# Kernel optimization log

Measured on AMD Instinct MI355X. Metric: run time of the kernel, lower is better.

## Reference

```python
import jax, jax.numpy as jnp
import numpy as np

NUM_HEADS = 16


def setup_inputs() -> dict:
    key = jax.random.key(0)
    ks = jax.random.split(key, 8)
    B, N, C = 2, 1024, 1024
    H, D = NUM_HEADS, C // NUM_HEADS
    Npast = 8192
    s = 0.02
    return {
        "x": jax.random.normal(ks[0], (B, N, C), jnp.float32),
        "past_k": jax.random.normal(ks[1], (B, H, Npast, D), jnp.float32),
        "past_v": jax.random.normal(ks[2], (B, H, Npast, D), jnp.float32),
        "qkv_w": jax.random.normal(ks[3], (3 * C, C), jnp.float32) * s,
        "qkv_b": jax.random.normal(ks[4], (3 * C,), jnp.float32) * s,
        "proj_w": jax.random.normal(ks[5], (C, C), jnp.float32) * s,
        "proj_b": jax.random.normal(ks[6], (C,), jnp.float32) * s,
        "cache_budget": 4096,
    }


def reference(x, past_k, past_v, qkv_w, qkv_b, proj_w, proj_b, cache_budget):
    B, N, C = x.shape
    H = NUM_HEADS
    D = C // H
    scale = D ** -0.5

    # fused QKV projection -> [3, B, H, N, D]
    qkv = (x @ qkv_w.T + qkv_b).reshape(B, N, 3, H, D).transpose(2, 0, 3, 1, 4)
    q, k, v = qkv[0], qkv[1], qkv[2]

    # use_cache path: anchor tokens = current-frame token count on first call
    num_anchor = N
    k = jnp.concatenate([past_k, k], axis=2)  # [B,H,Ntot,D]
    v = jnp.concatenate([past_v, v], axis=2)
    Ntot = k.shape[2]

    # eviction: mean cosine-similarity scoring over candidate (non-anchor) keys.
    # mean_j cos(k_i, k_j) == khat_i . mean_j(khat_j) -- O(N*D), no NxN matrix.
    num_keep = cache_budget - num_anchor
    cand_k = k[:, :, num_anchor:, :]  # [B,H,Ncand,D]
    khat = cand_k / (jnp.linalg.norm(cand_k, axis=-1, keepdims=True) + 1e-6)
    mean_dir = khat.mean(axis=2, keepdims=True)
    mean_scores = (khat * mean_dir).sum(-1)  # [B,H,Ncand]
    # keep the least-redundant tokens (lowest mean similarity)
    _, top_idx = jax.lax.top_k(-mean_scores, num_keep)  # [B,H,num_keep]
    top_idx = jnp.sort(top_idx, axis=-1)
    avg_scores = mean_scores.mean()

    anchor_idx = jnp.broadcast_to(jnp.arange(num_anchor)[None, None, :], (B, H, num_anchor))
    keep_idx = jnp.concatenate([anchor_idx, top_idx + num_anchor], axis=2)  # [B,H,budget]
    gidx = keep_idx[..., None]
    k_new = jnp.take_along_axis(k, jnp.broadcast_to(gidx, (B, H, cache_budget, D)), axis=2)
    v_new = jnp.take_along_axis(v, jnp.broadcast_to(gidx, (B, H, cache_budget, D)), axis=2)

    # SDPA
    logits = jnp.einsum("bhqd,bhkd->bhqk", q, k_new) * scale
    attn = jax.nn.softmax(logits, axis=-1)
    o = jnp.einsum("bhqk,bhkd->bhqd", attn, v_new)
    o = o.transpose(0, 2, 1, 3).reshape(B, N, C)
    out = o @ proj_w.T + proj_b
    return out, k_new, v_new, avg_scores
```

## Files before the change

### kernel.cpp

```cpp
#include <hip/hip_runtime.h>
#include <hip/hip_bf16.h>
#include <math.h>

#define BB 2
#define HH 16
#define NN 1024
#define CC 1024
#define DD 64
#define NPAST 8192
#define NANCH 1024
#define CBUD 4096
#define NKEEP 3072
#define NCAND 8192
#define BH 32

#define TILEB 16384

#define OUT_SZ   (BB*NN*CC)
#define KNEW_OFF ((size_t)OUT_SZ)
#define KNEW_SZ  ((size_t)BH*CBUD*DD)
#define VNEW_OFF (KNEW_OFF + KNEW_SZ)
#define AVG_OFF  (VNEW_OFF + KNEW_SZ)

#define WS_KF   ((size_t)0)
#define WS_VF   ((size_t)2097152)
#define WS_VTS  ((size_t)0)
#define WS_XT   ((size_t)4194304)
#define WS_OT   ((size_t)4194304)
#define WS_WQVT ((size_t)5242880)
#define WS_WPT  ((size_t)5242880)
#define WS_QB   ((size_t)6291456)
#define WS_MD   ((size_t)7340032)
#define WS_SC   ((size_t)7342080)
#define WS_BS   ((size_t)7604224)
#define WS_SEL  ((size_t)7604288)
#define WS_MDP  ((size_t)7702592)
#define WS_BSP  ((size_t)7718976)
#define WS_KTS  ((size_t)7719232)

typedef __attribute__((ext_vector_type(8))) short short8;
typedef __attribute__((ext_vector_type(4))) float f32x4;

typedef unsigned int __attribute__((address_space(3))) lds_uint;
typedef unsigned int __attribute__((address_space(1))) glb_uint;

__device__ __forceinline__ void gload16(const void* g, void* l) {
    __builtin_amdgcn_global_load_lds((const glb_uint*)g, (lds_uint*)l, 16, 0, 0);
}

__device__ inline unsigned short f2bf(float f) {
    unsigned u = __float_as_uint(f);
    unsigned r = (u + 0x7FFFu + ((u >> 16) & 1u)) >> 16;
    return (unsigned short)r;
}
__device__ inline unsigned cvtpk(float a, float b) {
    __hip_bfloat162 h = __float22bfloat162_rn(make_float2(a, b));
    return *reinterpret_cast<unsigned*>(&h);
}
__device__ __forceinline__ float fexp2(float x) {
#if __has_builtin(__builtin_amdgcn_exp2f)
    return __builtin_amdgcn_exp2f(x);
#else
    return exp2f(x);
#endif
}

__global__ __launch_bounds__(256) void kf_conv(const float* __restrict__ x,
                                               const float* __restrict__ qw,
                                               const float* __restrict__ bias,
                                               float* __restrict__ ws,
                                               unsigned short* __restrict__ xt,
                                               unsigned short* __restrict__ wqvt)
{
    __shared__ float As[2][16][68];
    __shared__ float Bs[2][16][68];
    int bid = blockIdx.x;
    int tid = threadIdx.x;

    if (bid >= 512) {
        int cb = bid - 512;
        int gid = (cb & 1023) * 256 + tid;
        int r = gid >> 7, k0 = (gid & 127) * 8;
        const float* src;
        unsigned short* dst;
        int srow;
        if (cb < 1024) { src = x;  dst = xt;   srow = r; }
        else           { src = qw; dst = wqvt; srow = (r < 1024) ? r : r + 1024; }
        float4 a = *(const float4*)&src[(size_t)srow * 1024 + k0];
        float4 b = *(const float4*)&src[(size_t)srow * 1024 + k0 + 4];
        uint4 u;
        u.x = cvtpk(a.x, a.y); u.y = cvtpk(a.z, a.w);
        u.z = cvtpk(b.x, b.y); u.w = cvtpk(b.z, b.w);
        size_t tile = (size_t)(r >> 7) * 16 + (k0 >> 6);
        int inner = (((r & 127) * 128 + (k0 & 63) * 2)) ^ ((r & 7) << 4);
        *(uint4*)((char*)dst + tile * TILEB + inner) = u;
        return;
    }

    int m0 = (bid >> 4) * 64;
    int n0 = (bid & 15) * 64;
    int tx = tid & 15, ty = tid >> 4;
    int lr = tid >> 2;
    int lk = (tid & 3) * 4;
    float acc[4][4] = {{0.f}};

    {
        float4 a = *(const float4*)&x[(size_t)(m0 + lr) * CC + lk];
        float4 b = *(const float4*)&qw[(size_t)(1024 + n0 + lr) * CC + lk];
        As[0][lk+0][lr] = a.x; As[0][lk+1][lr] = a.y; As[0][lk+2][lr] = a.z; As[0][lk+3][lr] = a.w;
        Bs[0][lk+0][lr] = b.x; Bs[0][lk+1][lr] = b.y; Bs[0][lk+2][lr] = b.z; Bs[0][lk+3][lr] = b.w;
    }
    __syncthreads();

    int cur = 0;
    for (int k0 = 0; k0 < CC; k0 += 16) {
        float4 a, b;
        bool more = (k0 + 16 < CC);
        if (more) {
            a = *(const float4*)&x[(size_t)(m0 + lr) * CC + k0 + 16 + lk];
            b = *(const float4*)&qw[(size_t)(1024 + n0 + lr) * CC + k0 + 16 + lk];
        }
        float tacc[4][4] = {{0.f}};
        #pragma unroll
        for (int kk = 0; kk < 16; ++kk) {
            float4 a4 = *(const float4*)&As[cur][kk][ty*4];
            float4 b4 = *(const float4*)&Bs[cur][kk][tx*4];
            float av[4] = {a4.x, a4.y, a4.z, a4.w};
            float bv[4] = {b4.x, b4.y, b4.z, b4.w};
            #pragma unroll
            for (int i = 0; i < 4; ++i)
                #pragma unroll
                for (int j = 0; j < 4; ++j)
                    tacc[i][j] += av[i] * bv[j];
        }
        #pragma unroll
        for (int i = 0; i < 4; ++i)
            #pragma unroll
            for (int j = 0; j < 4; ++j)
                acc[i][j] += tacc[i][j];
        if (more) {
            As[cur^1][lk+0][lr] = a.x; As[cur^1][lk+1][lr] = a.y;
            As[cur^1][lk+2][lr] = a.z; As[cur^1][lk+3][lr] = a.w;
            Bs[cur^1][lk+0][lr] = b.x; Bs[cur^1][lk+1][lr] = b.y;
            Bs[cur^1][lk+2][lr] = b.z; Bs[cur^1][lk+3][lr] = b.w;
        }
        __syncthreads();
        cur ^= 1;
    }

    int cn0 = n0 + tx * 4;
    int h = cn0 >> 6, dd0 = cn0 & 63;
    float4 b4 = *(const float4*)&bias[1024 + cn0];
    float* kf = ws + WS_KF;
    #pragma unroll
    for (int i = 0; i < 4; ++i) {
        int m = m0 + ty * 4 + i;
        int b2 = m >> 10, n = m & 1023;
        float4 t;
        t.x = acc[i][0] + b4.x; t.y = acc[i][1] + b4.y;
        t.z = acc[i][2] + b4.z; t.w = acc[i][3] + b4.w;
        *(float4*)&kf[(((size_t)b2*HH + h)*NN + n)*DD + dd0] = t;
    }
}

template<int MODE>
__global__ __launch_bounds__(256) void mfma_gemm(const unsigned short* __restrict__ At,
                                                 const unsigned short* __restrict__ Bt,
                                                 const float* __restrict__ bias,
                                                 float* __restrict__ outp)
{
    __shared__ char lds[131072];
    int tid = threadIdx.x;
    int w = tid >> 6, lane = tid & 63;
    int g = lane >> 4, r16 = lane & 15;
    int wr = w >> 1, wc = w & 1;
    int bm = blockIdx.y, bn = blockIdx.x;
    const int KB = 16;
    const float QSCL = 0.125f * 1.44269504089f;

    f32x4 acc[4][4];
    #pragma unroll
    for (int i = 0; i < 4; ++i)
        #pragma unroll
        for (int j = 0; j < 4; ++j) acc[i][j] = 0.f;

    const char* Abase = (const char*)At + (size_t)bm * KB * TILEB;
    const char* Bbase = (const char*)Bt + (size_t)bn * KB * TILEB;

    #pragma unroll
    for (int i = 0; i < 4; ++i) {
        gload16(Abase + (size_t)w*4096 + i*1024 + lane*16, lds + w*4096 + i*1024);
        gload16(Bbase + (size_t)w*4096 + i*1024 + lane*16, lds + TILEB + w*4096 + i*1024);
    }
    asm volatile("s_waitcnt vmcnt(0)" ::: "memory");
    __syncthreads();

    int cur = 0;
    for (int kb = 0; kb < KB; ++kb) {
        char* Acur = lds + cur * (2*TILEB);
        char* Bcur = Acur + TILEB;
        if (kb + 1 < KB) {
            char* Anxt = lds + (cur ^ 1) * (2*TILEB);
            char* Bnxt = Anxt + TILEB;
            const char* an = Abase + (size_t)(kb+1)*TILEB + w*4096;
            const char* bsrc = Bbase + (size_t)(kb+1)*TILEB + w*4096;
            #pragma unroll
            for (int i = 0; i < 4; ++i) {
                gload16(an + i*1024 + lane*16, Anxt + w*4096 + i*1024);
                gload16(bsrc + i*1024 + lane*16, Bnxt + w*4096 + i*1024);
            }
        }
        short8 a0[4], a1[4], b0[4], b1[4];
        #pragma unroll
        for (int mi = 0; mi < 4; ++mi) {
            int row = wr*64 + mi*16 + r16;
            int sw = (row & 7) << 4;
            a0[mi] = *(const short8*)(Acur + ((row*128 + g*16) ^ sw));
            a1[mi] = *(const short8*)(Acur + ((row*128 + 64 + g*16) ^ sw));
        }
        #pragma unroll
        for (int ni = 0; ni < 4; ++ni) {
            int row = wc*64 + ni*16 + r16;
            int sw = (row & 7) << 4;
            b0[ni] = *(const short8*)(Bcur + ((row*128 + g*16) ^ sw));
            b1[ni] = *(const short8*)(Bcur + ((row*128 + 64 + g*16) ^ sw));
        }
        __builtin_amdgcn_s_setprio(1);
        #pragma unroll
        for (int mi = 0; mi < 4; ++mi)
            #pragma unroll
            for (int ni = 0; ni < 4; ++ni) {
                acc[mi][ni] = __builtin_amdgcn_mfma_f32_16x16x32_bf16(a0[mi], b0[ni], acc[mi][ni], 0, 0, 0);
                acc[mi][ni] = __builtin_amdgcn_mfma_f32_16x16x32_bf16(a1[mi], b1[ni], acc[mi][ni], 0, 0, 0);
            }
        __builtin_amdgcn_s_setprio(0);
        asm volatile("s_waitcnt vmcnt(0)" ::: "memory");
        __syncthreads();
        cur ^= 1;
    }

    int nq = bn*128 + wc*64;
    float bv[4];
    #pragma unroll
    for (int ni = 0; ni < 4; ++ni) {
        int n = nq + ni*16 + r16;
        bv[ni] = (MODE == 0) ? bias[(n < 1024) ? n : (n + 1024)] : bias[n];
    }
    #pragma unroll
    for (int mi = 0; mi < 4; ++mi) {
        #pragma unroll
        for (int rr = 0; rr < 4; ++rr) {
            int ml = wr*64 + mi*16 + 4*g + rr;
            int mg = bm*128 + ml;
            int bb = mg >> 10, tok = mg & 1023;
            #pragma unroll
            for (int ni = 0; ni < 4; ++ni) {
                int n = nq + ni*16 + r16;
                float v = acc[mi][ni][rr] + bv[ni];
                if (MODE == 0) {
                    if (n < 1024) {
                        unsigned short* qb = (unsigned short*)(outp + WS_QB);
                        int hh = n >> 6, d = n & 63;
                        qb[(((size_t)bb*16 + hh)*1024 + tok)*64 + d] = f2bf(v * QSCL);
                    } else {
                        float* vf = outp + WS_VF;
                        int hh = (n - 1024) >> 6, d = n & 63;
                        vf[(((size_t)bb*16 + hh)*1024 + tok)*64 + d] = v;
                    }
                } else {
                    outp[(size_t)mg*1024 + n] = v;
                }
            }
        }
    }
}

__global__ __launch_bounds__(256) void meandir_part(const float* __restrict__ past_k,
                                                    float* __restrict__ ws)
{
    int bh = blockIdx.x, seg = blockIdx.y, tid = threadIdx.x;
    const float* kpast = past_k + (size_t)bh * NPAST * DD;
    const float* knew  = ws + WS_KF + (size_t)bh * NN * DD;
    float dir[64];
    #pragma unroll
    for (int i = 0; i < 64; ++i) dir[i] = 0.f;

    int j0 = seg * 1024;
    for (int jj = tid; jj < 1024; jj += 256) {
        int pos = NANCH + j0 + jj;
        const float* row = (pos < NPAST) ? (kpast + (size_t)pos * DD)
                                         : (knew + (size_t)(pos - NPAST) * DD);
        float v[64]; float ss = 0.f;
        #pragma unroll
        for (int g = 0; g < 16; ++g) {
            float4 t = *(const float4*)&row[g*4];
            v[4*g]=t.x; v[4*g+1]=t.y; v[4*g+2]=t.z; v[4*g+3]=t.w;
            ss += t.x*t.x + t.y*t.y + t.z*t.z + t.w*t.w;
        }
        float inv = 1.0f / (sqrtf(ss) + 1e-6f);
        #pragma unroll
        for (int i = 0; i < 64; ++i) dir[i] += v[i] * inv;
    }
    #pragma unroll
    for (int i = 0; i < 64; ++i)
        for (int off = 32; off; off >>= 1) dir[i] += __shfl_xor(dir[i], off);

    __shared__ float sdir[4][64];
    int lane = tid & 63, wid = tid >> 6;
    if (lane == 0) {
        #pragma unroll
        for (int i = 0; i < 64; ++i) sdir[wid][i] = dir[i];
    }
    __syncthreads();
    if (tid < 64) {
        float s = sdir[0][tid] + sdir[1][tid] + sdir[2][tid] + sdir[3][tid];
        ws[WS_MDP + ((size_t)bh*8 + seg)*DD + tid] = s;
    }
}

__global__ __launch_bounds__(256) void scores_part(const float* __restrict__ past_k,
                                                   float* __restrict__ ws)
{
    __shared__ float md[64];
    __shared__ float sred[4];
    int bh = blockIdx.x, seg = blockIdx.y, tid = threadIdx.x;
    if (tid < 64) {
        float s = 0.f;
        #pragma unroll
        for (int sg = 0; sg < 8; ++sg)
            s += ws[WS_MDP + ((size_t)bh*8 + sg)*DD + tid];
        md[tid] = s * (1.0f / (float)NCAND);
    }
    __syncthreads();
    const float* kpast = past_k + (size_t)bh * NPAST * DD;
    const float* knew  = ws + WS_KF + (size_t)bh * NN * DD;
    float ssum = 0.f;
    int j0 = seg * 1024;
    for (int jj = tid; jj < 1024; jj += 256) {
        int j = j0 + jj;
        int pos = NANCH + j;
        const float* row = (pos < NPAST) ? (kpast + (size_t)pos * DD)
                                         : (knew + (size_t)(pos - NPAST) * DD);
        float ss = 0.f, dp = 0.f;
        #pragma unroll
        for (int g = 0; g < 16; ++g) {
            float4 t = *(const float4*)&row[g*4];
            ss += t.x*t.x + t.y*t.y + t.z*t.z + t.w*t.w;
            dp += t.x*md[4*g] + t.y*md[4*g+1] + t.z*md[4*g+2] + t.w*md[4*g+3];
        }
        float sc = dp / (sqrtf(ss) + 1e-6f);
        ws[WS_SC + (size_t)bh*NCAND + j] = sc;
        ssum += sc;
    }
    for (int off = 32; off; off >>= 1) ssum += __shfl_xor(ssum, off);
    int lane = tid & 63, wid = tid >> 6;
    if (lane == 0) sred[wid] = ssum;
    __syncthreads();
    if (tid == 0)
        ws[WS_BSP + (size_t)bh*8 + seg] = sred[0] + sred[1] + sred[2] + sred[3];
}

__global__ __launch_bounds__(1024) void topk_k(float* __restrict__ ws, int* __restrict__ sel,
                                               float* __restrict__ dout)
{
    __shared__ unsigned keys[NCAND];
    __shared__ int hist[256];
    __shared__ int red[16];
    __shared__ int red2[16];
    __shared__ float fred[16];
    __shared__ int bcast;
    __shared__ unsigned bbyte;
    int bh = blockIdx.x, tid = threadIdx.x;
    int lane = tid & 63, wid = tid >> 6;

    if (bh == 0) {
        float v = (tid < 256) ? ws[WS_BSP + tid] : 0.f;
        for (int off = 32; off; off >>= 1) v += __shfl_xor(v, off);
        if (lane == 0) fred[wid] = v;
        __syncthreads();
        if (tid == 0) {
            float s = 0.f;
            for (int i = 0; i < 16; ++i) s += fred[i];
            dout[AVG_OFF] = s * (1.0f / ((float)BH * (float)NCAND));
        }
        __syncthreads();
    }

    for (int j = tid; j < NCAND; j += 1024) {
        unsigned u = __float_as_uint(ws[WS_SC + (size_t)bh*NCAND + j]);
        u ^= (u & 0x80000000u) ? 0xFFFFFFFFu : 0x80000000u;
        keys[j] = u;
    }
    __syncthreads();

    int rem = NKEEP;
    unsigned prefix = 0;
    #pragma unroll
    for (int pass = 0; pass < 4; ++pass) {
        int shift = 24 - 8*pass;
        if (tid < 256) hist[tid] = 0;
        __syncthreads();
        unsigned himask = (pass == 0) ? 0u : (0xFFFFFFFFu << (shift + 8));
        for (int j = tid; j < NCAND; j += 1024) {
            unsigned k = keys[j];
            if ((k & himask) == prefix)
                atomicAdd(&hist[(k >> shift) & 255], 1);
        }
        __syncthreads();
        if (tid == 0) {
            int cum = 0, b = 0;
            for (; b < 255; ++b) {
                if (rem <= cum + hist[b]) break;
                cum += hist[b];
            }
            bcast = cum;
            bbyte = (unsigned)b;
        }
        __syncthreads();
        rem -= bcast;
        prefix |= (bbyte << shift);
        __syncthreads();
    }
    unsigned T = prefix;

    {
        int cnt = 0;
        for (int j = tid; j < NCAND; j += 1024) cnt += (int)(keys[j] < T);
        for (int off = 32; off; off >>= 1) cnt += __shfl_xor(cnt, off);
        if (lane == 0) red[wid] = cnt;
        __syncthreads();
        if (tid == 0) { int c = 0; for (int i = 0; i < 16; ++i) c += red[i]; bcast = c; }
        __syncthreads();
    }
    int c_less = bcast;
    int ttie = NKEEP - c_less;

    int base = tid * 8;
    unsigned kv[8]; int lcnt = 0, ecnt = 0;
    #pragma unroll
    for (int i = 0; i < 8; ++i) {
        kv[i] = keys[base + i];
        lcnt += (int)(kv[i] < T);
        ecnt += (int)(kv[i] == T);
    }
    int li = lcnt, ei = ecnt;
    for (int off = 1; off < 64; off <<= 1) {
        int tl = __shfl_up(li, off);
        int te = __shfl_up(ei, off);
        if (lane >= off) { li += tl; ei += te; }
    }
    __syncthreads();
    if (lane == 63) { red[wid] = li; red2[wid] = ei; }
    __syncthreads();
    int lb = 0, eb = 0;
    for (int w = 0; w < wid; ++w) { lb += red[w]; eb += red2[w]; }
    lb += li - lcnt; eb += ei - ecnt;
    #pragma unroll
    for (int i = 0; i < 8; ++i) {
        bool less = kv[i] < T, eq = kv[i] == T;
        if (less || (eq && eb < ttie)) {
            int pos = lb + (eb < ttie ? eb : ttie);
            sel[(size_t)bh*NKEEP + pos] = base + i;
        }
        lb += (int)less; eb += (int)eq;
    }
}

__global__ __launch_bounds__(256) void gather_k(const float* __restrict__ past_k,
                                                const float* __restrict__ past_v,
                                                const float* __restrict__ ws,
                                                const int* __restrict__ sel,
                                                float* __restrict__ dout)
{
    int gid = blockIdx.x * 256 + threadIdx.x;
    int row = gid >> 4, lane = gid & 15;
    int bh = row >> 12, r = row & 4095;
    int pos = (r < NANCH) ? r : (NANCH + sel[(size_t)bh*NKEEP + (r - NANCH)]);
    const float *kr, *vr;
    if (pos < NPAST) {
        kr = past_k + ((size_t)bh*NPAST + pos) * DD;
        vr = past_v + ((size_t)bh*NPAST + pos) * DD;
    } else {
        kr = ws + WS_KF + ((size_t)bh*NN + (pos - NPAST)) * DD;
        vr = ws + WS_VF + ((size_t)bh*NN + (pos - NPAST)) * DD;
    }
    float4 kq = *(const float4*)&kr[lane*4];
    float4 vq = *(const float4*)&vr[lane*4];
    *(float4*)&dout[KNEW_OFF + ((size_t)bh*CBUD + r)*DD + lane*4] = kq;
    *(float4*)&dout[VNEW_OFF + ((size_t)bh*CBUD + r)*DD + lane*4] = vq;
}

__global__ __launch_bounds__(256) void vtrans_conv(const float* __restrict__ dout,
                                                   unsigned short* __restrict__ vt,
                                                   const float* __restrict__ pw,
                                                   unsigned short* __restrict__ wpt,
                                                   unsigned short* __restrict__ ktp,
                                                   int nkblk)
{
    int bid = blockIdx.x;
    if (bid >= 2048 && bid < 2048 + nkblk) {
        int bid2 = bid - 2048;
        int bh = bid2 >> 6, kt = bid2 & 63;
        int tid = threadIdx.x;
        int r = tid >> 2, c4 = (tid & 3) * 16;
        const float* kn = dout + KNEW_OFF + ((size_t)bh*CBUD + kt*64 + r)*DD + c4;
        float4 f0 = *(const float4*)&kn[0];
        float4 f1 = *(const float4*)&kn[4];
        float4 f2 = *(const float4*)&kn[8];
        float4 f3 = *(const float4*)&kn[12];
        uint4 u0, u1;
        u0.x = cvtpk(f0.x,f0.y); u0.y = cvtpk(f0.z,f0.w);
        u0.z = cvtpk(f1.x,f1.y); u0.w = cvtpk(f1.z,f1.w);
        u1.x = cvtpk(f2.x,f2.y); u1.y = cvtpk(f2.z,f2.w);
        u1.z = cvtpk(f3.x,f3.y); u1.w = cvtpk(f3.z,f3.w);
        size_t tbase = ((size_t)bh*64 + kt) * 8192;
        int sw = (r & 7) << 4;
        *(uint4*)((char*)ktp + tbase + ((r*128 + c4*2)      ^ sw)) = u0;
        *(uint4*)((char*)ktp + tbase + ((r*128 + c4*2 + 16) ^ sw)) = u1;
        return;
    }
    if (bid >= 2048 + nkblk) {
        int gid = (bid - 2048 - nkblk) * 256 + threadIdx.x;
        int r = gid >> 7, k0 = (gid & 127) * 8;
        float4 a = *(const float4*)&pw[(size_t)r * 1024 + k0];
        float4 b = *(const float4*)&pw[(size_t)r * 1024 + k0 + 4];
        uint4 u;
        u.x = cvtpk(a.x, a.y); u.y = cvtpk(a.z, a.w);
        u.z = cvtpk(b.x, b.y); u.w = cvtpk(b.z, b.w);
        size_t tile = (size_t)(r >> 7) * 16 + (k0 >> 6);
        int inner = (((r & 127) * 128 + (k0 & 63) * 2)) ^ ((r & 7) << 4);
        *(uint4*)((char*)wpt + tile * TILEB + inner) = u;
        return;
    }
    __shared__ unsigned short S[64][65];
    int bh = bid >> 6, kt = bid & 63;
    int c0 = kt * 64;
    int tid = threadIdx.x;
    int r = tid >> 2, c4 = (tid & 3) * 16;
    const float* src = dout + VNEW_OFF + ((size_t)bh*CBUD + c0 + r)*DD + c4;
    #pragma unroll
    for (int i = 0; i < 4; ++i) {
        float4 f = *(const float4*)&src[i*4];
        S[r][c4 + i*4 + 0] = f2bf(f.x);
        S[r][c4 + i*4 + 1] = f2bf(f.y);
        S[r][c4 + i*4 + 2] = f2bf(f.z);
        S[r][c4 + i*4 + 3] = f2bf(f.w);
    }
    __syncthreads();
    int d = r, k4 = c4;
    uint4 u0, u1;
    u0.x = (unsigned)S[k4+0][d] | ((unsigned)S[k4+1][d] << 16);
    u0.y = (unsigned)S[k4+2][d] | ((unsigned)S[k4+3][d] << 16);
    u0.z = (unsigned)S[k4+4][d] | ((unsigned)S[k4+5][d] << 16);
    u0.w = (unsigned)S[k4+6][d] | ((unsigned)S[k4+7][d] << 16);
    u1.x = (unsigned)S[k4+8][d] | ((unsigned)S[k4+9][d] << 16);
    u1.y = (unsigned)S[k4+10][d] | ((unsigned)S[k4+11][d] << 16);
    u1.z = (unsigned)S[k4+12][d] | ((unsigned)S[k4+13][d] << 16);
    u1.w = (unsigned)S[k4+14][d] | ((unsigned)S[k4+15][d] << 16);
    size_t tbase = ((size_t)bh*64 + kt) * 8192;
    int sw = (d & 7) << 4;
    *(uint4*)((char*)vt + tbase + ((d*128 + k4*2)      ^ sw)) = u0;
    *(uint4*)((char*)vt + tbase + ((d*128 + k4*2 + 16) ^ sw)) = u1;
}

template<int KTS>
__global__ __launch_bounds__(256) void attn_mfma(const unsigned short* __restrict__ qb,
                                                 const float* __restrict__ dout,
                                                 const unsigned short* __restrict__ vt,
                                                 const unsigned short* __restrict__ ktp,
                                                 unsigned short* __restrict__ ot)
{
    __shared__ char kls[2][2][8192];
    __shared__ char vls[2][2][8192];
    __shared__ char pls[4][2048];

    int orig = blockIdx.x;
    int bid = (orig & 7) * 64 + (orig >> 3);
    int bh = bid >> 4, qt = bid & 15;
    int b = bh >> 4, h = bh & 15;
    int tid = threadIdx.x;
    int w = tid >> 6, lane = tid & 63;
    int g = lane >> 4, r16 = lane & 15;
    int q0 = qt * 64 + w * 16;

    const unsigned short* qrow = qb + ((size_t)bh*NN + q0 + r16) * DD;
    short8 qa0 = *(const short8*)&qrow[8*g];
    short8 qa1 = *(const short8*)&qrow[32 + 8*g];

    const float* kf = dout + KNEW_OFF + (size_t)bh * CBUD * DD;
    const char* vtt = (const char*)vt + (size_t)bh * 64 * 8192;
    const char* ktt = (const char*)ktp + (size_t)bh * 64 * 8192;
    char* plw = pls[w];
    int psw = (r16 & 7) << 4;

    int ro[8];
    #pragma unroll
    for (int t4 = 0; t4 < 4; ++t4) {
        int row = 16*t4 + r16;
        ro[2*t4]   = (row*128 + g*16) ^ psw;
        ro[2*t4+1] = (row*128 + 64 + g*16) ^ psw;
    }
    int pwo[4];
    #pragma unroll
    for (int t4 = 0; t4 < 4; ++t4)
        pwo[t4] = (r16*128 + (16*t4 + 4*g)*2) ^ psw;
    int pro0 = (r16*128 + 16*g) ^ psw;
    int pro1 = (r16*128 + 64 + 16*g) ^ psw;

    int srA = tid >> 3, srB = srA + 32;
    int scb = (tid & 7) * 16;
    int d0  = scb >> 1;
    int sdA = (srA*128 + scb) ^ ((srA & 7) << 4);
    int sdB = (srB*128 + scb) ^ ((srB & 7) << 4);

    f32x4 accd[4];
    #pragma unroll
    for (int dt = 0; dt < 4; ++dt) accd[dt] = 0.f;
    float lsum = 0.f;
// ... 12 lines not shown
            #pragma unroll
            for (int hh = 0; hh < 2; ++hh) {
                const float* ksA = kf + ((size_t)hh*64 + srA) * DD + d0;
                const float* ksB = kf + ((size_t)hh*64 + srB) * DD + d0;
                float4 a0 = *(const float4*)ksA, a1 = *(const float4*)(ksA + 4);
                float4 b0 = *(const float4*)ksB, b1 = *(const float4*)(ksB + 4);
                uint4 kuA, kuB;
                kuA.x = cvtpk(a0.x,a0.y); kuA.y = cvtpk(a0.z,a0.w);
                kuA.z = cvtpk(a1.x,a1.y); kuA.w = cvtpk(a1.z,a1.w);
                kuB.x = cvtpk(b0.x,b0.y); kuB.y = cvtpk(b0.z,b0.w);
                kuB.z = cvtpk(b1.x,b1.y); kuB.w = cvtpk(b1.z,b1.w);
                *(uint4*)&kls[0][hh][sdA] = kuA;
                *(uint4*)&kls[0][hh][sdB] = kuB;
            }
        }
    }
    __syncthreads();

    int cur = 0;
    for (int t = 0; t < 32; ++t) {
        float4 na0[2], na1[2], nb0[2], nb1[2];
        bool more = (t + 1 < 32);
        if (more) {
            int nt = 2*t + 2;
            const char* vsrc = vtt + (size_t)nt*8192;
            gload16(vsrc + tid*16,         vls[cur^1][0] + tid*16);
            gload16(vsrc + 4096 + tid*16,  vls[cur^1][0] + 4096 + tid*16);
            gload16(vsrc + 8192 + tid*16,  vls[cur^1][1] + tid*16);
            gload16(vsrc + 12288 + tid*16, vls[cur^1][1] + 4096 + tid*16);
            if (KTS) {
                const char* ksrc = ktt + (size_t)nt*8192;
                gload16(ksrc + tid*16,         kls[cur^1][0] + tid*16);
                gload16(ksrc + 4096 + tid*16,  kls[cur^1][0] + 4096 + tid*16);
                gload16(ksrc + 8192 + tid*16,  kls[cur^1][1] + tid*16);
                gload16(ksrc + 12288 + tid*16, kls[cur^1][1] + 4096 + tid*16);
            } else {
                #pragma unroll
                for (int hh = 0; hh < 2; ++hh) {
                    const float* ksA = kf + ((size_t)(nt+hh)*64 + srA) * DD + d0;
                    const float* ksB = kf + ((size_t)(nt+hh)*64 + srB) * DD + d0;
                    na0[hh] = *(const float4*)ksA; na1[hh] = *(const float4*)(ksA + 4);
                    nb0[hh] = *(const float4*)ksB; nb1[hh] = *(const float4*)(ksB + 4);
                }
            }
        }

        #pragma unroll
        for (int hh = 0; hh < 2; ++hh) {
            const char* kb = kls[cur][hh];
            f32x4 sacc[4];
            #pragma unroll
            for (int t4 = 0; t4 < 4; ++t4) sacc[t4] = 0.f;
            __builtin_amdgcn_s_setprio(1);
            #pragma unroll
            for (int t4 = 0; t4 < 4; ++t4) {
                short8 ka0 = *(const short8*)(kb + ro[2*t4]);
                short8 ka1 = *(const short8*)(kb + ro[2*t4+1]);
                sacc[t4] = __builtin_amdgcn_mfma_f32_16x16x32_bf16(ka0, qa0, sacc[t4], 0, 0, 0);
                sacc[t4] = __builtin_amdgcn_mfma_f32_16x16x32_bf16(ka1, qa1, sacc[t4], 0, 0, 0);
            }
            __builtin_amdgcn_s_setprio(0);

            float p[4][4];
            float ps = 0.f;
            #pragma unroll
            for (int t4 = 0; t4 < 4; ++t4) {
                p[t4][0] = fexp2(sacc[t4][0]);
                p[t4][1] = fexp2(sacc[t4][1]);
                p[t4][2] = fexp2(sacc[t4][2]);
                p[t4][3] = fexp2(sacc[t4][3]);
                ps += (p[t4][0] + p[t4][1]) + (p[t4][2] + p[t4][3]);
            }
            lsum += ps;
            #pragma unroll
            for (int t4 = 0; t4 < 4; ++t4) {
                uint2 u;
                u.x = cvtpk(p[t4][0], p[t4][1]);
                u.y = cvtpk(p[t4][2], p[t4][3]);
                *(uint2*)&plw[pwo[t4]] = u;
            }

            short8 pa0 = *(const short8*)&plw[pro0];
            short8 pa1 = *(const short8*)&plw[pro1];
            const char* vb = vls[cur][hh];
            __builtin_amdgcn_s_setprio(1);
            #pragma unroll
            for (int dt = 0; dt < 4; ++dt) {
                short8 vb0 = *(const short8*)(vb + ro[2*dt]);
                short8 vb1 = *(const short8*)(vb + ro[2*dt+1]);
                accd[dt] = __builtin_amdgcn_mfma_f32_16x16x32_bf16(pa0, vb0, accd[dt], 0, 0, 0);
                accd[dt] = __builtin_amdgcn_mfma_f32_16x16x32_bf16(pa1, vb1, accd[dt], 0, 0, 0);
            }
            __builtin_amdgcn_s_setprio(0);
        }

        if (more && !KTS) {
            #pragma unroll
            for (int hh = 0; hh < 2; ++hh) {
                uint4 kuA, kuB;
                kuA.x = cvtpk(na0[hh].x, na0[hh].y); kuA.y = cvtpk(na0[hh].z, na0[hh].w);
                kuA.z = cvtpk(na1[hh].x, na1[hh].y); kuA.w = cvtpk(na1[hh].z, na1[hh].w);
                kuB.x = cvtpk(nb0[hh].x, nb0[hh].y); kuB.y = cvtpk(nb0[hh].z, nb0[hh].w);
                kuB.z = cvtpk(nb1[hh].x, nb1[hh].y); kuB.w = cvtpk(nb1[hh].z, nb1[hh].w);
                *(uint4*)&kls[cur^1][hh][sdA] = kuA;
                *(uint4*)&kls[cur^1][hh][sdB] = kuB;
            }
        }
        __syncthreads();
        cur ^= 1;
    }

    lsum += __shfl_xor(lsum, 16);
    lsum += __shfl_xor(lsum, 32);
    float ivl = 1.0f / lsum;
    float iq[4];
    #pragma unroll
    for (int rr = 0; rr < 4; ++rr) iq[rr] = __shfl(ivl, 20*g + rr);
    #pragma unroll
    for (int dt = 0; dt < 4; ++dt) {
        #pragma unroll
        for (int rr = 0; rr < 4; ++rr) {
            int q = q0 + 4*g + rr;
            int mrow = b*1024 + q;
            int d = dt*16 + r16;
            size_t tile = (size_t)(mrow >> 7) * 16 + h;
            int inner = ((mrow & 127)*128 + d*2) ^ ((mrow & 7) << 4);
            *(unsigned short*)((char*)ot + tile*TILEB + inner) = f2bf(accd[dt][rr] * iq[rr]);
        }
    }
}

extern "C" void kernel_launch(void* const* d_in, const int* in_sizes, int n_in,
                              void* d_out, int out_size, void* d_ws, size_t ws_size,
                              hipStream_t stream)
{
    (void)in_sizes; (void)n_in; (void)out_size;
    const float* x      = (const float*)d_in[0];
    const float* past_k = (const float*)d_in[1];
    const float* past_v = (const float*)d_in[2];
    const float* qkv_w  = (const float*)d_in[3];
    const float* qkv_b  = (const float*)d_in[4];
    const float* proj_w = (const float*)d_in[5];
    const float* proj_b = (const float*)d_in[6];
    float* out = (float*)d_out;
    float* ws  = (float*)d_ws;
    int*   sel = (int*)(ws + WS_SEL);
    unsigned short* xt   = (unsigned short*)(ws + WS_XT);
    unsigned short* wqvt = (unsigned short*)(ws + WS_WQVT);
    unsigned short* wpt  = (unsigned short*)(ws + WS_WPT);
    unsigned short* qbp  = (unsigned short*)(ws + WS_QB);
    unsigned short* vtp  = (unsigned short*)(ws + WS_VTS);
    unsigned short* otp  = (unsigned short*)(ws + WS_OT);
    unsigned short* ktp  = (unsigned short*)(ws + WS_KTS);

    int use_kts = (ws_size >= (size_t)(WS_KTS + 4194304) * sizeof(float)) ? 1 : 0;
    int nkblk = use_kts ? 2048 : 0;

    kf_conv<<<2560, 256, 0, stream>>>(x, qkv_w, qkv_b, ws, xt, wqvt);
    mfma_gemm<0><<<dim3(16, 16), 256, 0, stream>>>(xt, wqvt, qkv_b, ws);
    meandir_part<<<dim3(32, 8), 256, 0, stream>>>(past_k, ws);
    scores_part<<<dim3(32, 8), 256, 0, stream>>>(past_k, ws);
    topk_k<<<32, 1024, 0, stream>>>(ws, sel, out);
    gather_k<<<8192, 256, 0, stream>>>(past_k, past_v, ws, sel, out);
    vtrans_conv<<<2048 + nkblk + 512, 256, 0, stream>>>(out, vtp, proj_w, wpt, ktp, nkblk);
    if (use_kts)
        attn_mfma<1><<<512, 256, 0, stream>>>(qbp, out, vtp, ktp, otp);
    else
        attn_mfma<0><<<512, 256, 0, stream>>>(qbp, out, vtp, ktp, otp);
    mfma_gemm<1><<<dim3(8, 16), 256, 0, stream>>>(otp, wpt, proj_b, out);
}
```

Measured before the change: 270.7 us.

## Fuse mean-direction into QKV kernels and merge gather with bf16 K/V transposes

Splits the mean-direction reduction in two. The past-key segments run as extra blocks in the conversion/K-projection kernel, and the new-key segment runs as extra blocks in the Q/V GEMM kernel, so the separate meandir launch goes away. A new gather_all kernel writes the fp32 k_new/v_new outputs and also emits the bf16 swizzled K tiles and transposed V tiles straight from registers, plus the proj weight conversion. This removes the reread of the gathered output in vtrans_conv. The new path needs a larger workspace and falls back to the old path otherwise. Co-scheduling different block types in one launch may cause load imbalance.

```diff
diff --git a/kernel.cpp b/kernel.cpp
--- a/kernel.cpp
+++ b/kernel.cpp
@@ -37,6 +37,7 @@
 #define WS_MDP  ((size_t)7702592)
 #define WS_BSP  ((size_t)7718976)
 #define WS_KTS  ((size_t)7719232)
+#define WS_VTS2 ((size_t)11913536)
 
 typedef __attribute__((ext_vector_type(8))) short short8;
 typedef __attribute__((ext_vector_type(4))) float f32x4;
@@ -70,12 +71,51 @@
                                                const float* __restrict__ bias,
                                                float* __restrict__ ws,
                                                unsigned short* __restrict__ xt,
-                                               unsigned short* __restrict__ wqvt)
+                                               unsigned short* __restrict__ wqvt,
+                                               const float* __restrict__ past_k)
 {
-    __shared__ float As[2][16][68];
-    __shared__ float Bs[2][16][68];
+    __shared__ char shm[17408];
     int bid = blockIdx.x;
     int tid = threadIdx.x;
+
+    if (bid >= 2560) {
+        int mb = bid - 2560;
+        int bh = mb / 7, seg = mb % 7;
+        const float* kpast = past_k + (size_t)bh * NPAST * DD;
+        float dir[64];
+        #pragma unroll
+        for (int i = 0; i < 64; ++i) dir[i] = 0.f;
+        int j0 = seg * 1024;
+        for (int jj = tid; jj < 1024; jj += 256) {
+            int pos = NANCH + j0 + jj;
+            const float* row = kpast + (size_t)pos * DD;
+            float v[64]; float ss = 0.f;
+            #pragma unroll
+            for (int g = 0; g < 16; ++g) {
+                float4 t = *(const float4*)&row[g*4];
+                v[4*g]=t.x; v[4*g+1]=t.y; v[4*g+2]=t.z; v[4*g+3]=t.w;
+                ss += t.x*t.x + t.y*t.y + t.z*t.z + t.w*t.w;
+            }
+            float inv = 1.0f / (sqrtf(ss) + 1e-6f);
+            #pragma unroll
+            for (int i = 0; i < 64; ++i) dir[i] += v[i] * inv;
+        }
+        #pragma unroll
+        for (int i = 0; i < 64; ++i)
+            for (int off = 32; off; off >>= 1) dir[i] += __shfl_xor(dir[i], off);
+        float* sdir = (float*)shm;
+        int lane = tid & 63, wid = tid >> 6;
+        if (lane == 0) {
+            #pragma unroll
+            for (int i = 0; i < 64; ++i) sdir[wid*64 + i] = dir[i];
+        }
+        __syncthreads();
+        if (tid < 64) {
+            float s = sdir[0*64+tid] + sdir[1*64+tid] + sdir[2*64+tid] + sdir[3*64+tid];
+            ws[WS_MDP + ((size_t)bh*8 + seg)*DD + tid] = s;
+        }
+        return;
+    }
 
     if (bid >= 512) {
         int cb = bid - 512;
@@ -97,6 +137,8 @@
         return;
     }
 
+    float (*As)[16][68] = (float(*)[16][68])shm;
+    float (*Bs)[16][68] = (float(*)[16][68])(shm + 8704);
     int m0 = (bid >> 4) * 64;
     int n0 = (bid & 15) * 64;
     int tx = tid & 15, ty = tid >> 4;
@@ -163,8 +205,152 @@
     }
 }
 
-template<int MODE>
-__global__ __launch_bounds__(256) void mfma_gemm(const unsigned short* __restrict__ At,
+__global__ __launch_bounds__(256) void qv_md(const unsigned short* __restrict__ At,
+                                             const unsigned short* __restrict__ Bt,
+                                             const float* __restrict__ bias,
+                                             float* __restrict__ outp)
+{
+    __shared__ char lds[131072];
+    int bid = blockIdx.x;
+    int tid = threadIdx.x;
+
+    if (bid >= 256) {
+        int bh = bid - 256;
+        const float* knew = outp + WS_KF + (size_t)bh * NN * DD;
+        float dir[64];
+        #pragma unroll
+        for (int i = 0; i < 64; ++i) dir[i] = 0.f;
+        for (int jj = tid; jj < 1024; jj += 256) {
+            const float* row = knew + (size_t)jj * DD;
+            float v[64]; float ss = 0.f;
+            #pragma unroll
+            for (int g = 0; g < 16; ++g) {
+                float4 t = *(const float4*)&row[g*4];
+                v[4*g]=t.x; v[4*g+1]=t.y; v[4*g+2]=t.z; v[4*g+3]=t.w;
+                ss += t.x*t.x + t.y*t.y + t.z*t.z + t.w*t.w;
+            }
+            float inv = 1.0f / (sqrtf(ss) + 1e-6f);
+            #pragma unroll
+            for (int i = 0; i < 64; ++i) dir[i] += v[i] * inv;
+        }
+        #pragma unroll
+        for (int i = 0; i < 64; ++i)
+            for (int off = 32; off; off >>= 1) dir[i] += __shfl_xor(dir[i], off);
+        float* sdir = (float*)lds;
+        int lane = tid & 63, wid = tid >> 6;
+        if (lane == 0) {
+            #pragma unroll
+            for (int i = 0; i < 64; ++i) sdir[wid*64 + i] = dir[i];
+        }
+        __syncthreads();
+        if (tid < 64) {
+            float s = sdir[0*64+tid] + sdir[1*64+tid] + sdir[2*64+tid] + sdir[3*64+tid];
+            outp[WS_MDP + ((size_t)bh*8 + 7)*DD + tid] = s;
+        }
+        return;
+    }
+
+    int w = tid >> 6, lane = tid & 63;
+    int g = lane >> 4, r16 = lane & 15;
+    int wr = w >> 1, wc = w & 1;
+    int bm = bid >> 4, bn = bid & 15;
+    const int KB = 16;
+    const float QSCL = 0.125f * 1.44269504089f;
+
+    f32x4 acc[4][4];
+    #pragma unroll
+    for (int i = 0; i < 4; ++i)
+        #pragma unroll
+        for (int j = 0; j < 4; ++j) acc[i][j] = 0.f;
+
+    const char* Abase = (const char*)At + (size_t)bm * KB * TILEB;
+    const char* Bbase = (const char*)Bt + (size_t)bn * KB * TILEB;
+
+    #pragma unroll
+    for (int i = 0; i < 4; ++i) {
+        gload16(Abase + (size_t)w*4096 + i*1024 + lane*16, lds + w*4096 + i*1024);
+        gload16(Bbase + (size_t)w*4096 + i*1024 + lane*16, lds + TILEB + w*4096 + i*1024);
+    }
+    asm volatile("s_waitcnt vmcnt(0)" ::: "memory");
+    __syncthreads();
+
+    int cur = 0;
+    for (int kb = 0; kb < KB; ++kb) {
+        char* Acur = lds + cur * (2*TILEB);
+        char* Bcur = Acur + TILEB;
+        if (kb + 1 < KB) {
+            char* Anxt = lds + (cur ^ 1) * (2*TILEB);
+            char* Bnxt = Anxt + TILEB;
+            const char* an = Abase + (size_t)(kb+1)*TILEB + w*4096;
+            const char* bsrc = Bbase + (size_t)(kb+1)*TILEB + w*4096;
+            #pragma unroll
+            for (int i = 0; i < 4; ++i) {
+                gload16(an + i*1024 + lane*16, Anxt + w*4096 + i*1024);
+                gload16(bsrc + i*1024 + lane*16, Bnxt + w*4096 + i*1024);
+            }
+        }
+        short8 a0[4], a1[4], b0[4], b1[4];
+        #pragma unroll
+        for (int mi = 0; mi < 4; ++mi) {
+            int row = wr*64 + mi*16 + r16;
+            int sw = (row & 7) << 4;
+            a0[mi] = *(const short8*)(Acur + ((row*128 + g*16) ^ sw));
+            a1[mi] = *(const short8*)(Acur + ((row*128 + 64 + g*16) ^ sw));
+        }
+        #pragma unroll
+        for (int ni = 0; ni < 4; ++ni) {
+            int row = wc*64 + ni*16 + r16;
+            int sw = (row & 7) << 4;
+            b0[ni] = *(const short8*)(Bcur + ((row*128 + g*16) ^ sw));
+            b1[ni] = *(const short8*)(Bcur + ((row*128 + 64 + g*16) ^ sw));
+        }
+        __builtin_amdgcn_s_setprio(1);
+        #pragma unroll
+        for (int mi = 0; mi < 4; ++mi)
+            #pragma unroll
+            for (int ni = 0; ni < 4; ++ni) {
+                acc[mi][ni] = __builtin_amdgcn_mfma_f32_16x16x32_bf16(a0[mi], b0[ni], acc[mi][ni], 0, 0, 0);
+                acc[mi][ni] = __builtin_amdgcn_mfma_f32_16x16x32_bf16(a1[mi], b1[ni], acc[mi][ni], 0, 0, 0);
+            }
+        __builtin_amdgcn_s_setprio(0);
+        asm volatile("s_waitcnt vmcnt(0)" ::: "memory");
+        __syncthreads();
+        cur ^= 1;
+    }
+
+    int nq = bn*128 + wc*64;
+    float bv[4];
+    #pragma unroll
+    for (int ni = 0; ni < 4; ++ni) {
+        int n = nq + ni*16 + r16;
+        bv[ni] = bias[(n < 1024) ? n : (n + 1024)];
+    }
+    #pragma unroll
+    for (int mi = 0; mi < 4; ++mi) {
+        #pragma unroll
+        for (int rr = 0; rr < 4; ++rr) {
+            int ml = wr*64 + mi*16 + 4*g + rr;
+            int mg = bm*128 + ml;
+            int bb = mg >> 10, tok = mg & 1023;
+            #pragma unroll
+            for (int ni = 0; ni < 4; ++ni) {
+                int n = nq + ni*16 + r16;
+                float v = acc[mi][ni][rr] + bv[ni];
+                if (n < 1024) {
+                    unsigned short* qb = (unsigned short*)(outp + WS_QB);
+                    int hh = n >> 6, d = n & 63;
+                    qb[(((size_t)bb*16 + hh)*1024 + tok)*64 + d] = f2bf(v * QSCL);
+                } else {
+                    float* vf = outp + WS_VF;
+                    int hh = (n - 1024) >> 6, d = n & 63;
+                    vf[(((size_t)bb*16 + hh)*1024 + tok)*64 + d] = v;
+                }
+            }
+        }
+    }
+}
+
+__global__ __launch_bounds__(256) void proj_mfma(const unsigned short* __restrict__ At,
                                                  const unsigned short* __restrict__ Bt,
                                                  const float* __restrict__ bias,
                                                  float* __restrict__ outp)
@@ -176,7 +362,6 @@
     int wr = w >> 1, wc = w & 1;
     int bm = blockIdx.y, bn = blockIdx.x;
     const int KB = 16;
-    const float QSCL = 0.125f * 1.44269504089f;
 
     f32x4 acc[4][4];
     #pragma unroll
@@ -242,79 +427,18 @@
     int nq = bn*128 + wc*64;
     float bv[4];
     #pragma unroll
-    for (int ni = 0; ni < 4; ++ni) {
-        int n = nq + ni*16 + r16;
-        bv[ni] = (MODE == 0) ? bias[(n < 1024) ? n : (n + 1024)] : bias[n];
-    }
+    for (int ni = 0; ni < 4; ++ni) bv[ni] = bias[nq + ni*16 + r16];
     #pragma unroll
     for (int mi = 0; mi < 4; ++mi) {
         #pragma unroll
         for (int rr = 0; rr < 4; ++rr) {
-            int ml = wr*64 + mi*16 + 4*g + rr;
-            int mg = bm*128 + ml;
-            int bb = mg >> 10, tok = mg & 1023;
+            int mg = bm*128 + wr*64 + mi*16 + 4*g + rr;
             #pragma unroll
             for (int ni = 0; ni < 4; ++ni) {
                 int n = nq + ni*16 + r16;
-                float v = acc[mi][ni][rr] + bv[ni];
-                if (MODE == 0) {
-                    if (n < 1024) {
-                        unsigned short* qb = (unsigned short*)(outp + WS_QB);
-                        int hh = n >> 6, d = n & 63;
-                        qb[(((size_t)bb*16 + hh)*1024 + tok)*64 + d] = f2bf(v * QSCL);
-                    } else {
-                        float* vf = outp + WS_VF;
-                        int hh = (n - 1024) >> 6, d = n & 63;
-                        vf[(((size_t)bb*16 + hh)*1024 + tok)*64 + d] = v;
-                    }
-                } else {
-                    outp[(size_t)mg*1024 + n] = v;
-                }
-            }
-        }
-    }
-}
-
-__global__ __launch_bounds__(256) void meandir_part(const float* __restrict__ past_k,
-                                                    float* __restrict__ ws)
-{
-    int bh = blockIdx.x, seg = blockIdx.y, tid = threadIdx.x;
-    const float* kpast = past_k + (size_t)bh * NPAST * DD;
-    const float* knew  = ws + WS_KF + (size_t)bh * NN * DD;
-    float dir[64];
-    #pragma unroll
-    for (int i = 0; i < 64; ++i) dir[i] = 0.f;
-
-    int j0 = seg * 1024;
-    for (int jj = tid; jj < 1024; jj += 256) {
-        int pos = NANCH + j0 + jj;
-        const float* row = (pos < NPAST) ? (kpast + (size_t)pos * DD)
-                                         : (knew + (size_t)(pos - NPAST) * DD);
-        float v[64]; float ss = 0.f;
-        #pragma unroll
-        for (int g = 0; g < 16; ++g) {
-            float4 t = *(const float4*)&row[g*4];
-            v[4*g]=t.x; v[4*g+1]=t.y; v[4*g+2]=t.z; v[4*g+3]=t.w;
-            ss += t.x*t.x + t.y*t.y + t.z*t.z + t.w*t.w;
-        }
-        float inv = 1.0f / (sqrtf(ss) + 1e-6f);
-        #pragma unroll
-        for (int i = 0; i < 64; ++i) dir[i] += v[i] * inv;
-    }
-    #pragma unroll
-    for (int i = 0; i < 64; ++i)
-        for (int off = 32; off; off >>= 1) dir[i] += __shfl_xor(dir[i], off);
-
-    __shared__ float sdir[4][64];
-    int lane = tid & 63, wid = tid >> 6;
-    if (lane == 0) {
-        #pragma unroll
-        for (int i = 0; i < 64; ++i) sdir[wid][i] = dir[i];
-    }
-    __syncthreads();
-    if (tid < 64) {
-        float s = sdir[0][tid] + sdir[1][tid] + sdir[2][tid] + sdir[3][tid];
-        ws[WS_MDP + ((size_t)bh*8 + seg)*DD + tid] = s;
+                outp[(size_t)mg*1024 + n] = acc[mi][ni][rr] + bv[ni];
+            }
+        }
     }
 }
 
@@ -464,6 +588,91 @@
         }
         lb += (int)less; eb += (int)eq;
     }
+}
+
+__global__ __launch_bounds__(256) void gather_all(const float* __restrict__ past_k,
+                                                  const float* __restrict__ past_v,
+                                                  const float* __restrict__ ws,
+                                                  const int* __restrict__ sel,
+                                                  float* __restrict__ dout,
+                                                  unsigned short* __restrict__ ktp,
+                                                  unsigned short* __restrict__ vtp2,
+                                                  const float* __restrict__ pw,
+                                                  unsigned short* __restrict__ wpt)
+{
+    __shared__ unsigned short S[64][65];
+    int bid = blockIdx.x;
+    int tid = threadIdx.x;
+
+    if (bid >= 2048) {
+        int gid = (bid - 2048) * 256 + tid;
+        int r = gid >> 7, k0 = (gid & 127) * 8;
+        float4 a = *(const float4*)&pw[(size_t)r * 1024 + k0];
+        float4 b = *(const float4*)&pw[(size_t)r * 1024 + k0 + 4];
+        uint4 u;
+        u.x = cvtpk(a.x, a.y); u.y = cvtpk(a.z, a.w);
+        u.z = cvtpk(b.x, b.y); u.w = cvtpk(b.z, b.w);
+        size_t tile = (size_t)(r >> 7) * 16 + (k0 >> 6);
+        int inner = (((r & 127) * 128 + (k0 & 63) * 2)) ^ ((r & 7) << 4);
+        *(uint4*)((char*)wpt + tile * TILEB + inner) = u;
+        return;
+    }
+
+    int bh = bid >> 6, kt = bid & 63;
+    int r = tid >> 2, c4 = (tid & 3) * 16;
+    int rr = kt * 64 + r;
+    int pos = (rr < NANCH) ? rr : (NANCH + sel[(size_t)bh*NKEEP + (rr - NANCH)]);
+    const float *kr, *vr;
+    if (pos < NPAST) {
+        kr = past_k + ((size_t)bh*NPAST + pos) * DD + c4;
+        vr = past_v + ((size_t)bh*NPAST + pos) * DD + c4;
+    } else {
+        kr = ws + WS_KF + ((size_t)bh*NN + (pos - NPAST)) * DD + c4;
+        vr = ws + WS_VF + ((size_t)bh*NN + (pos - NPAST)) * DD + c4;
+    }
+    float4 k0 = *(const float4*)&kr[0], k1 = *(const float4*)&kr[4];
+    float4 k2 = *(const float4*)&kr[8], k3 = *(const float4*)&kr[12];
+    float4 v0 = *(const float4*)&vr[0], v1 = *(const float4*)&vr[4];
+    float4 v2 = *(const float4*)&vr[8], v3 = *(const float4*)&vr[12];
+
+    float* kd = dout + KNEW_OFF + ((size_t)bh*CBUD + rr)*DD + c4;
+    float* vd = dout + VNEW_OFF + ((size_t)bh*CBUD + rr)*DD + c4;
+    *(float4*)&kd[0] = k0; *(float4*)&kd[4] = k1;
+    *(float4*)&kd[8] = k2; *(float4*)&kd[12] = k3;
+    *(float4*)&vd[0] = v0; *(float4*)&vd[4] = v1;
+    *(float4*)&vd[8] = v2; *(float4*)&vd[12] = v3;
+
+    {
+        uint4 u0, u1;
+        u0.x = cvtpk(k0.x,k0.y); u0.y = cvtpk(k0.z,k0.w);
+        u0.z = cvtpk(k1.x,k1.y); u0.w = cvtpk(k1.z,k1.w);
+        u1.x = cvtpk(k2.x,k2.y); u1.y = cvtpk(k2.z,k2.w);
+        u1.z = cvtpk(k3.x,k3.y); u1.w = cvtpk(k3.z,k3.w);
+        size_t tbase = ((size_t)bh*64 + kt) * 8192;
+        int sw = (r & 7) << 4;
+        *(uint4*)((char*)ktp + tbase + ((r*128 + c4*2)      ^ sw)) = u0;
+        *(uint4*)((char*)ktp + tbase + ((r*128 + c4*2 + 16) ^ sw)) = u1;
+    }
+
+    S[r][c4+0]=f2bf(v0.x); S[r][c4+1]=f2bf(v0.y); S[r][c4+2]=f2bf(v0.z); S[r][c4+3]=f2bf(v0.w);
+    S[r][c4+4]=f2bf(v1.x); S[r][c4+5]=f2bf(v1.y); S[r][c4+6]=f2bf(v1.z); S[r][c4+7]=f2bf(v1.w);
+    S[r][c4+8]=f2bf(v2.x); S[r][c4+9]=f2bf(v2.y); S[r][c4+10]=f2bf(v2.z); S[r][c4+11]=f2bf(v2.w);
+    S[r][c4+12]=f2bf(v3.x); S[r][c4+13]=f2bf(v3.y); S[r][c4+14]=f2bf(v3.z); S[r][c4+15]=f2bf(v3.w);
+    __syncthreads();
+    int d = r, k4 = c4;
+    uint4 u0, u1;
+    u0.x = (unsigned)S[k4+0][d] | ((unsigned)S[k4+1][d] << 16);
+    u0.y = (unsigned)S[k4+2][d] | ((unsigned)S[k4+3][d] << 16);
+    u0.z = (unsigned)S[k4+4][d] | ((unsigned)S[k4+5][d] << 16);
+    u0.w = (unsigned)S[k4+6][d] | ((unsigned)S[k4+7][d] << 16);
+    u1.x = (unsigned)S[k4+8][d] | ((unsigned)S[k4+9][d] << 16);
+    u1.y = (unsigned)S[k4+10][d] | ((unsigned)S[k4+11][d] << 16);
+    u1.z = (unsigned)S[k4+12][d] | ((unsigned)S[k4+13][d] << 16);
+    u1.w = (unsigned)S[k4+14][d] | ((unsigned)S[k4+15][d] << 16);
+    size_t tbase = ((size_t)bh*64 + kt) * 8192;
+    int sw = (d & 7) << 4;
+    *(uint4*)((char*)vtp2 + tbase + ((d*128 + k4*2)      ^ sw)) = u0;
+    *(uint4*)((char*)vtp2 + tbase + ((d*128 + k4*2 + 16) ^ sw)) = u1;
 }
 
 __global__ __launch_bounds__(256) void gather_k(const float* __restrict__ past_k,
@@ -782,20 +991,26 @@
     unsigned short* vtp  = (unsigned short*)(ws + WS_VTS);
     unsigned short* otp  = (unsigned short*)(ws + WS_OT);
     unsigned short* ktp  = (unsigned short*)(ws + WS_KTS);
-
+    unsigned short* vtp2 = (unsigned short*)(ws + WS_VTS2);
+
+    int tierA = (ws_size >= (size_t)(WS_VTS2 + 4194304) * sizeof(float)) ? 1 : 0;
     int use_kts = (ws_size >= (size_t)(WS_KTS + 4194304) * sizeof(float)) ? 1 : 0;
-    int nkblk = use_kts ? 2048 : 0;
-
-    kf_conv<<<2560, 256, 0, stream>>>(x, qkv_w, qkv_b, ws, xt, wqvt);
-    mfma_gemm<0><<<dim3(16, 16), 256, 0, stream>>>(xt, wqvt, qkv_b, ws);
-    meandir_part<<<dim3(32, 8), 256, 0, stream>>>(past_k, ws);
+
+    kf_conv<<<2784, 256, 0, stream>>>(x, qkv_w, qkv_b, ws, xt, wqvt, past_k);
+    qv_md<<<288, 256, 0, stream>>>(xt, wqvt, qkv_b, ws);
     scores_part<<<dim3(32, 8), 256, 0, stream>>>(past_k, ws);
     topk_k<<<32, 1024, 0, stream>>>(ws, sel, out);
-    gather_k<<<8192, 256, 0, stream>>>(past_k, past_v, ws, sel, out);
-    vtrans_conv<<<2048 + nkblk + 512, 256, 0, stream>>>(out, vtp, proj_w, wpt, ktp, nkblk);
-    if (use_kts)
-        attn_mfma<1><<<512, 256, 0, stream>>>(qbp, out, vtp, ktp, otp);
-    else
-        attn_mfma<0><<<512, 256, 0, stream>>>(qbp, out, vtp, ktp, otp);
-    mfma_gemm<1><<<dim3(8, 16), 256, 0, stream>>>(otp, wpt, proj_b, out);
-}
+    if (tierA) {
+        gather_all<<<2560, 256, 0, stream>>>(past_k, past_v, ws, sel, out, ktp, vtp2, proj_w, wpt);
+        attn_mfma<1><<<512, 256, 0, stream>>>(qbp, out, vtp2, ktp, otp);
+    } else {
+        int nkblk = use_kts ? 2048 : 0;
+        gather_k<<<8192, 256, 0, stream>>>(past_k, past_v, ws, sel, out);
+        vtrans_conv<<<2048 + nkblk + 512, 256, 0, stream>>>(out, vtp, proj_w, wpt, ktp, nkblk);
+        if (use_kts)
+            attn_mfma<1><<<512, 256, 0, stream>>>(qbp, out, vtp, ktp, otp);
+        else
+            attn_mfma<0><<<512, 256, 0, stream>>>(qbp, out, vtp, ktp, otp);
+    }
+    proj_mfma<<<dim3(8, 16), 256, 0, stream>>>(otp, wpt, proj_b, out);
+}
```

New measurement: 284.1 us. 4.9% more time.

## Fuse KV gather with bf16 K/V tiling and proj weight conversion

Applied to the files above, without the earlier changes.

Adds a gather_all kernel that gathers the selected K/V rows, writes the fp32 k_new/v_new outputs, and in the same pass emits swizzled bf16 K tiles and LDS-transposed bf16 V tiles, plus converts proj_w. This replaces the separate gather_k and vtrans_conv launches, so the gathered K/V no longer has to be re-read from global memory. It uses a separate workspace region for the transposed V and only runs when the workspace is large enough; otherwise the old path remains.

```diff
diff --git a/kernel.cpp b/kernel.cpp
--- a/kernel.cpp
+++ b/kernel.cpp
@@ -37,6 +37,7 @@
 #define WS_MDP  ((size_t)7702592)
 #define WS_BSP  ((size_t)7718976)
 #define WS_KTS  ((size_t)7719232)
+#define WS_VTS2 ((size_t)11913536)
 
 typedef __attribute__((ext_vector_type(8))) short short8;
 typedef __attribute__((ext_vector_type(4))) float f32x4;
@@ -464,6 +465,91 @@
         }
         lb += (int)less; eb += (int)eq;
     }
+}
+
+__global__ __launch_bounds__(256) void gather_all(const float* __restrict__ past_k,
+                                                  const float* __restrict__ past_v,
+                                                  const float* __restrict__ ws,
+                                                  const int* __restrict__ sel,
+                                                  float* __restrict__ dout,
+                                                  unsigned short* __restrict__ ktp,
+                                                  unsigned short* __restrict__ vtp2,
+                                                  const float* __restrict__ pw,
+                                                  unsigned short* __restrict__ wpt)
+{
+    __shared__ unsigned short S[64][65];
+    int bid = blockIdx.x;
+    int tid = threadIdx.x;
+
+    if (bid >= 2048) {
+        int gid = (bid - 2048) * 256 + tid;
+        int r = gid >> 7, k0 = (gid & 127) * 8;
+        float4 a = *(const float4*)&pw[(size_t)r * 1024 + k0];
+        float4 b = *(const float4*)&pw[(size_t)r * 1024 + k0 + 4];
+        uint4 u;
+        u.x = cvtpk(a.x, a.y); u.y = cvtpk(a.z, a.w);
+        u.z = cvtpk(b.x, b.y); u.w = cvtpk(b.z, b.w);
+        size_t tile = (size_t)(r >> 7) * 16 + (k0 >> 6);
+        int inner = (((r & 127) * 128 + (k0 & 63) * 2)) ^ ((r & 7) << 4);
+        *(uint4*)((char*)wpt + tile * TILEB + inner) = u;
+        return;
+    }
+
+    int bh = bid >> 6, kt = bid & 63;
+    int r = tid >> 2, c4 = (tid & 3) * 16;
+    int rr = kt * 64 + r;
+    int pos = (rr < NANCH) ? rr : (NANCH + sel[(size_t)bh*NKEEP + (rr - NANCH)]);
+    const float *kr, *vr;
+    if (pos < NPAST) {
+        kr = past_k + ((size_t)bh*NPAST + pos) * DD + c4;
+        vr = past_v + ((size_t)bh*NPAST + pos) * DD + c4;
+    } else {
+        kr = ws + WS_KF + ((size_t)bh*NN + (pos - NPAST)) * DD + c4;
+        vr = ws + WS_VF + ((size_t)bh*NN + (pos - NPAST)) * DD + c4;
+    }
+    float4 k0 = *(const float4*)&kr[0], k1 = *(const float4*)&kr[4];
+    float4 k2 = *(const float4*)&kr[8], k3 = *(const float4*)&kr[12];
+    float4 v0 = *(const float4*)&vr[0], v1 = *(const float4*)&vr[4];
+    float4 v2 = *(const float4*)&vr[8], v3 = *(const float4*)&vr[12];
+
+    float* kd = dout + KNEW_OFF + ((size_t)bh*CBUD + rr)*DD + c4;
+    float* vd = dout + VNEW_OFF + ((size_t)bh*CBUD + rr)*DD + c4;
+    *(float4*)&kd[0] = k0; *(float4*)&kd[4] = k1;
+    *(float4*)&kd[8] = k2; *(float4*)&kd[12] = k3;
+    *(float4*)&vd[0] = v0; *(float4*)&vd[4] = v1;
+    *(float4*)&vd[8] = v2; *(float4*)&vd[12] = v3;
+
+    {
+        uint4 u0, u1;
+        u0.x = cvtpk(k0.x,k0.y); u0.y = cvtpk(k0.z,k0.w);
+        u0.z = cvtpk(k1.x,k1.y); u0.w = cvtpk(k1.z,k1.w);
+        u1.x = cvtpk(k2.x,k2.y); u1.y = cvtpk(k2.z,k2.w);
+        u1.z = cvtpk(k3.x,k3.y); u1.w = cvtpk(k3.z,k3.w);
+        size_t tbase = ((size_t)bh*64 + kt) * 8192;
+        int sw = (r & 7) << 4;
+        *(uint4*)((char*)ktp + tbase + ((r*128 + c4*2)      ^ sw)) = u0;
+        *(uint4*)((char*)ktp + tbase + ((r*128 + c4*2 + 16) ^ sw)) = u1;
+    }
+
+    S[r][c4+0]=f2bf(v0.x); S[r][c4+1]=f2bf(v0.y); S[r][c4+2]=f2bf(v0.z); S[r][c4+3]=f2bf(v0.w);
+    S[r][c4+4]=f2bf(v1.x); S[r][c4+5]=f2bf(v1.y); S[r][c4+6]=f2bf(v1.z); S[r][c4+7]=f2bf(v1.w);
+    S[r][c4+8]=f2bf(v2.x); S[r][c4+9]=f2bf(v2.y); S[r][c4+10]=f2bf(v2.z); S[r][c4+11]=f2bf(v2.w);
+    S[r][c4+12]=f2bf(v3.x); S[r][c4+13]=f2bf(v3.y); S[r][c4+14]=f2bf(v3.z); S[r][c4+15]=f2bf(v3.w);
+    __syncthreads();
+    int d = r, k4 = c4;
+    uint4 u0, u1;
+    u0.x = (unsigned)S[k4+0][d] | ((unsigned)S[k4+1][d] << 16);
+    u0.y = (unsigned)S[k4+2][d] | ((unsigned)S[k4+3][d] << 16);
+    u0.z = (unsigned)S[k4+4][d] | ((unsigned)S[k4+5][d] << 16);
+    u0.w = (unsigned)S[k4+6][d] | ((unsigned)S[k4+7][d] << 16);
+    u1.x = (unsigned)S[k4+8][d] | ((unsigned)S[k4+9][d] << 16);
+    u1.y = (unsigned)S[k4+10][d] | ((unsigned)S[k4+11][d] << 16);
+    u1.z = (unsigned)S[k4+12][d] | ((unsigned)S[k4+13][d] << 16);
+    u1.w = (unsigned)S[k4+14][d] | ((unsigned)S[k4+15][d] << 16);
+    size_t tbase = ((size_t)bh*64 + kt) * 8192;
+    int sw = (d & 7) << 4;
+    *(uint4*)((char*)vtp2 + tbase + ((d*128 + k4*2)      ^ sw)) = u0;
+    *(uint4*)((char*)vtp2 + tbase + ((d*128 + k4*2 + 16) ^ sw)) = u1;
 }
 
 __global__ __launch_bounds__(256) void gather_k(const float* __restrict__ past_k,
@@ -782,20 +868,27 @@
     unsigned short* vtp  = (unsigned short*)(ws + WS_VTS);
     unsigned short* otp  = (unsigned short*)(ws + WS_OT);
     unsigned short* ktp  = (unsigned short*)(ws + WS_KTS);
-
+    unsigned short* vtp2 = (unsigned short*)(ws + WS_VTS2);
+
+    int tierA = (ws_size >= (size_t)(WS_VTS2 + 4194304) * sizeof(float)) ? 1 : 0;
     int use_kts = (ws_size >= (size_t)(WS_KTS + 4194304) * sizeof(float)) ? 1 : 0;
-    int nkblk = use_kts ? 2048 : 0;
 
     kf_conv<<<2560, 256, 0, stream>>>(x, qkv_w, qkv_b, ws, xt, wqvt);
     mfma_gemm<0><<<dim3(16, 16), 256, 0, stream>>>(xt, wqvt, qkv_b, ws);
     meandir_part<<<dim3(32, 8), 256, 0, stream>>>(past_k, ws);
     scores_part<<<dim3(32, 8), 256, 0, stream>>>(past_k, ws);
     topk_k<<<32, 1024, 0, stream>>>(ws, sel, out);
-    gather_k<<<8192, 256, 0, stream>>>(past_k, past_v, ws, sel, out);
-    vtrans_conv<<<2048 + nkblk + 512, 256, 0, stream>>>(out, vtp, proj_w, wpt, ktp, nkblk);
-    if (use_kts)
-        attn_mfma<1><<<512, 256, 0, stream>>>(qbp, out, vtp, ktp, otp);
-    else
-        attn_mfma<0><<<512, 256, 0, stream>>>(qbp, out, vtp, ktp, otp);
+    if (tierA) {
+        gather_all<<<2560, 256, 0, stream>>>(past_k, past_v, ws, sel, out, ktp, vtp2, proj_w, wpt);
+        attn_mfma<1><<<512, 256, 0, stream>>>(qbp, out, vtp2, ktp, otp);
+    } else {
+        int nkblk = use_kts ? 2048 : 0;
+        gather_k<<<8192, 256, 0, stream>>>(past_k, past_v, ws, sel, out);
+        vtrans_conv<<<2048 + nkblk + 512, 256, 0, stream>>>(out, vtp, proj_w, wpt, ktp, nkblk);
+        if (use_kts)
+            attn_mfma<1><<<512, 256, 0, stream>>>(qbp, out, vtp, ktp, otp);
+        else
+            attn_mfma<0><<<512, 256, 0, stream>>>(qbp, out, vtp, ktp, otp);
+    }
     mfma_gemm<1><<<dim3(8, 16), 256, 0, stream>>>(otp, wpt, proj_b, out);
 }
```

Result: no change. 273.8 us (+1.1%).
